# Performance work log

Measured on AMD Instinct MI355X. Metric: run time of the kernel, lower is better.

The kernel has to match this reference:

```python
import jax, jax.numpy as jnp
import numpy as np

N_NODES = 100000
N_EDGES = 1600000
N_FEAT = 165
HIDDEN = 128
N_CLASSES = 2
NEG_SLOPE = 0.2


def setup_inputs() -> dict:
    key = jax.random.key(0)
    ks = jax.random.split(key, 16)
    s = 0.05
    return {
        'x': jax.random.normal(ks[0], (N_NODES, N_FEAT), jnp.float32),
        'edge_src': jax.random.randint(ks[1], (N_EDGES,), 0, N_NODES, jnp.int32),
        'edge_dst': jax.random.randint(ks[2], (N_EDGES,), 0, N_NODES, jnp.int32),
        'W1l': jax.random.normal(ks[3], (N_FEAT, HIDDEN), jnp.float32) * s,
        'b1l': jnp.zeros((HIDDEN,), jnp.float32),
        'W1r': jax.random.normal(ks[4], (N_FEAT, HIDDEN), jnp.float32) * s,
        'b1r': jnp.zeros((HIDDEN,), jnp.float32),
        'att1': jax.random.normal(ks[5], (HIDDEN,), jnp.float32) * s,
        'bias1': jnp.zeros((HIDDEN,), jnp.float32),
        'W2l': jax.random.normal(ks[6], (HIDDEN, N_CLASSES), jnp.float32) * s,
        'b2l': jnp.zeros((N_CLASSES,), jnp.float32),
        'W2r': jax.random.normal(ks[7], (HIDDEN, N_CLASSES), jnp.float32) * s,
        'b2r': jnp.zeros((N_CLASSES,), jnp.float32),
        'att2': jax.random.normal(ks[8], (N_CLASSES,), jnp.float32) * s,
        'bias2': jnp.zeros((N_CLASSES,), jnp.float32),
    }


def gatv2_conv(x, src, dst, Wl, bl, Wr, br, att, bias, n_nodes):
    # PyG GATv2Conv, heads=1: x_l for source/message, x_r for target
    xl = x @ Wl + bl            # [N, D_out]
    xr = x @ Wr + br            # [N, D_out]
    e = jax.nn.leaky_relu(xl[src] + xr[dst], NEG_SLOPE)  # [E, D_out]
    score = e @ att             # [E]
    # segment softmax over destination nodes (stable)
    m = jax.ops.segment_max(score, dst, num_segments=n_nodes)
    a = jnp.exp(score - m[dst])
    denom = jax.ops.segment_sum(a, dst, num_segments=n_nodes)
    alpha = a / denom[dst]      # [E]
    out = jax.ops.segment_sum(alpha[:, None] * xl[src], dst, num_segments=n_nodes)
    return out + bias


def reference(x, edge_src, edge_dst, W1l, b1l, W1r, b1r, att1, bias1,
              W2l, b2l, W2r, b2r, att2, bias2):
    n = x.shape[0]
    # GATv2Conv adds self loops by default; every node has >=1 incoming edge
    loops = jnp.arange(n, dtype=edge_src.dtype)
    src = jnp.concatenate([edge_src, loops])
    dst = jnp.concatenate([edge_dst, loops])
    h = gatv2_conv(x, src, dst, W1l, b1l, W1r, b1r, att1, bias1, n)
    h = jax.nn.relu(h)
    # F.dropout with training=False is identity (eval mode)
    out = gatv2_conv(h, src, dst, W2l, b2l, W2r, b2r, att2, bias2, n)
    return out
```

## Files before the change

### kernel.cpp

```cpp
#include <hip/hip_runtime.h>
#include <hip/hip_bf16.h>

#define N_NODES 100000
#define NPAD 100032
#define N_EDGES 1600000
#define ETOT (N_EDGES + N_NODES)
#define NFEAT 165
#define KP 192
#define HID 128
#define NCLS 2
#define NEG 0.2f

#define NBUCK 391
#define CHUNK 16384
#define NCHUNK 104

typedef short bf16x8 __attribute__((ext_vector_type(8)));
typedef float f32x4 __attribute__((ext_vector_type(4)));

#define OFF_FLAG 0
#define OFF_W 16
#define WO_ATT1 42496
#define WO_BIAS1 42624
#define WO_W2L 42752
#define WO_B2L 43008
#define WO_W2R 43010
#define WO_B2R 43266
#define WO_ATT2 43268
#define WO_BIAS2 43270

#define OFF_XB   43392
#define OFF_WT   (OFF_XB + NPAD * KP / 2)
#define OFF_BCAT (OFF_WT + 256 * KP / 2)
#define OFF_XLB  (OFF_BCAT + 256)
#define OFF_XRB  (OFF_XLB + NPAD * HID / 2)
#define OFF_PAIRS (OFF_XRB + NPAD * HID / 2)
#define OFF_CSR  (OFF_PAIRS + 2 * ETOT)
#define OFF_ROWPTR (OFF_CSR + ETOT)
#define OFF_S    (OFF_ROWPTR + N_NODES + 8)
#define OFF_XL2  (OFF_S + NBUCK * NCHUNK + 8)
#define OFF_XR2  (OFF_XL2 + N_NODES * NCLS)
#define OFF_H    (OFF_XR2 + N_NODES * NCLS)
#define OFF_DL   (OFF_H + N_NODES * HID)
#define OFF_DR   (OFF_DL + NPAD)

__device__ __forceinline__ float bload16(unsigned short u) {
    return __uint_as_float(((unsigned)u) << 16);
}

__device__ __forceinline__ float lrelu(float v) {
    return fmaf(0.4f, fabsf(v), 0.6f * v);
}

__device__ __forceinline__ void unpack8(uint4 q, float* f) {
    f[0] = __uint_as_float(q.x << 16); f[1] = __uint_as_float(q.x & 0xffff0000u);
    f[2] = __uint_as_float(q.y << 16); f[3] = __uint_as_float(q.y & 0xffff0000u);
    f[4] = __uint_as_float(q.z << 16); f[5] = __uint_as_float(q.z & 0xffff0000u);
    f[6] = __uint_as_float(q.w << 16); f[7] = __uint_as_float(q.w & 0xffff0000u);
}

__device__ __forceinline__ unsigned short f2b(float f) {
    __hip_bfloat16 b = __float2bfloat16(f);
    return *(unsigned short*)&b;
}

__device__ __forceinline__ unsigned detect_flag(const unsigned short* x16, int lane) {
    unsigned short hh = x16[lane];
    unsigned e = (hh >> 7) & 0xFF;
    bool pl = ((hh & 0x7FFF) == 0) || (e >= 100 && e <= 140);
    unsigned long long m = __ballot(pl);
    return (__popcll(m) >= 52) ? 1u : 0u;
}

#define PREP_WT 49152
#define PREP_BC (PREP_WT + 256)
#define PREP_TOT (PREP_BC + 776)
#define PREP_BLKS ((PREP_TOT + 255) / 256)
__global__ void __launch_bounds__(256) k_prep_hist(
        const int* __restrict__ edst, int* __restrict__ bh,
        const unsigned short* __restrict__ x16,
        const void* W1l, const void* b1l, const void* W1r, const void* b1r,
        const void* att1, const void* bias1, const void* W2l, const void* b2l,
        const void* W2r, const void* b2r, const void* att2, const void* bias2,
        unsigned* __restrict__ flagp, unsigned short* __restrict__ wt,
        float* __restrict__ bcat, float* __restrict__ wb) {
    __shared__ int hist[NBUCK];
    if (blockIdx.x < NCHUNK) {
        for (int i = threadIdx.x; i < NBUCK; i += 256) hist[i] = 0;
        __syncthreads();
        int base = blockIdx.x * CHUNK;
        for (int i = threadIdx.x; i < CHUNK; i += 256) {
            int e = base + i;
            if (e >= ETOT) break;
            int d = (e < N_EDGES) ? edst[e] : (e - N_EDGES);
            atomicAdd(&hist[d >> 8], 1);
        }
        __syncthreads();
        for (int b = threadIdx.x; b < NBUCK; b += 256)
            bh[b * NCHUNK + blockIdx.x] = hist[b];
        return;
    }
    int lane = threadIdx.x & 63;
    unsigned isbf = detect_flag(x16, lane);
    int i = (blockIdx.x - NCHUNK) * 256 + threadIdx.x;
    if (i == 0) *flagp = isbf;
    if (i >= PREP_TOT) return;
    if (i < PREP_WT) {
        int n = i / KP, k = i - n * KP;
        unsigned short v = 0;
        if (k < NFEAT) {
            const void* src = (n < HID) ? W1l : W1r;
            size_t off = (size_t)k * HID + (n & (HID - 1));
            v = isbf ? ((const unsigned short*)src)[off]
                     : f2b(((const float*)src)[off]);
        }
        wt[i] = v;
    } else if (i < PREP_BC) {
        int n = i - PREP_WT;
        const void* src = (n < HID) ? b1l : b1r;
        int off = n & (HID - 1);
        bcat[n] = isbf ? bload16(((const unsigned short*)src)[off])
                       : ((const float*)src)[off];
    } else {
        int j = i - PREP_BC;
        const void* src; int off; int dst;
        if      (j < 128) { src = att1;  off = j;       dst = WO_ATT1 + j; }
        else if (j < 256) { src = bias1; off = j - 128; dst = WO_BIAS1 + (j - 128); }
        else if (j < 512) { src = W2l;   off = j - 256; dst = WO_W2L + (j - 256); }
        else if (j < 514) { src = b2l;   off = j - 512; dst = WO_B2L + (j - 512); }
        else if (j < 770) { src = W2r;   off = j - 514; dst = WO_W2R + (j - 514); }
        else if (j < 772) { src = b2r;   off = j - 770; dst = WO_B2R + (j - 770); }
        else if (j < 774) { src = att2;  off = j - 772; dst = WO_ATT2 + (j - 772); }
        else              { src = bias2; off = j - 774; dst = WO_BIAS2 + (j - 774); }
        wb[dst] = isbf ? bload16(((const unsigned short*)src)[off])
                       : ((const float*)src)[off];
    }
}

__global__ void __launch_bounds__(512) k_pa_scan(int* __restrict__ S,
                                                 int* __restrict__ rowptr) {
    __shared__ int lds[512];
    const int TOT4 = (NBUCK * NCHUNK) / 4;
    int t = threadIdx.x;
    int b4 = t * 20;
    uint4* S4 = (uint4*)S;
    int sum = 0;
    for (int k = 0; k < 20; k++) {
        int i = b4 + k;
        if (i < TOT4) {
            uint4 v = S4[i];
            sum += (int)(v.x + v.y + v.z + v.w);
        }
    }
    lds[t] = sum;
    __syncthreads();
    for (int off = 1; off < 512; off <<= 1) {
        int v = lds[t];
        if (t >= off) v += lds[t - off];
        __syncthreads();
        lds[t] = v;
        __syncthreads();
    }
    int carry = (t == 0) ? 0 : lds[t - 1];
    for (int k = 0; k < 20; k++) {
        int i = b4 + k;
        if (i < TOT4) {
            uint4 v = S4[i];
            uint4 o;
            o.x = carry; carry += v.x;
            o.y = carry; carry += v.y;
            o.z = carry; carry += v.z;
            o.w = carry; carry += v.w;
            S4[i] = o;
        }
    }
    if (t == 0) rowptr[N_NODES] = ETOT;
}

__global__ void __launch_bounds__(256) k_pa_scatter(const int* __restrict__ esrc,
                                                    const int* __restrict__ edst,
                                                    const int* __restrict__ S,
                                                    int2* __restrict__ pairs) {
    __shared__ int cur[NBUCK];
    for (int i = threadIdx.x; i < NBUCK; i += 256)
        cur[i] = S[i * NCHUNK + blockIdx.x];
    __syncthreads();
    int base = blockIdx.x * CHUNK;
    for (int i = threadIdx.x; i < CHUNK; i += 256) {
        int e = base + i;
        if (e >= ETOT) break;
        int s = (e < N_EDGES) ? esrc[e] : (e - N_EDGES);
        int d = (e < N_EDGES) ? edst[e] : (e - N_EDGES);
        int p = atomicAdd(&cur[d >> 8], 1);
        pairs[p] = make_int2(s, d);
    }
}

__global__ void __launch_bounds__(256) k_bsort(const int* __restrict__ S,
                                               const int2* __restrict__ pairs,
                                               int* __restrict__ rowptr,
                                               int* __restrict__ csr) {
    __shared__ int hist[256];
    __shared__ int cur[256];
    int b = blockIdx.x, t = threadIdx.x;
    int beg = S[b * NCHUNK];
    int end = (b == NBUCK - 1) ? ETOT : S[(b + 1) * NCHUNK];
    hist[t] = 0;
    __syncthreads();
    for (int j = beg + t; j < end; j += 256)
        atomicAdd(&hist[pairs[j].y & 255], 1);
    __syncthreads();
    for (int off = 1; off < 256; off <<= 1) {
        int v = hist[t];
        if (t >= off) v += hist[t - off];
        __syncthreads();
        hist[t] = v;
        __syncthreads();
    }
    int excl = (t == 0) ? 0 : hist[t - 1];
    int node = b * 256 + t;
    if (node < N_NODES) rowptr[node] = beg + excl;
    cur[t] = beg + excl;
    __syncthreads();
    for (int j = beg + t; j < end; j += 256) {
        int2 pr = pairs[j];
        int p = atomicAdd(&cur[pr.y & 255], 1);
        csr[p] = pr.x;
    }
}

#define XS_STRIDE 200
__global__ void __launch_bounds__(256) k_gemm1_mfma(
        const void* __restrict__ x,
        const unsigned* __restrict__ flagp,
        const unsigned short* __restrict__ wt,
        const float* __restrict__ bcat,
        const float* __restrict__ attp,
        __hip_bfloat16* __restrict__ xlb,
        __hip_bfloat16* __restrict__ xrb,
        float* __restrict__ dl,
        float* __restrict__ dr) {
    __shared__ unsigned short xs[64 * XS_STRIDE];
    __shared__ float dpart[4][64];
    int tid = threadIdx.x;
    int wave = tid >> 6, lane = tid & 63;
    int quad = lane >> 4, li = lane & 15;
    int node0 = blockIdx.x * 64;
    unsigned isbf = *flagp;
    const float* xf = (const float*)x;
    const unsigned short* x16 = (const unsigned short*)x;

    for (int i = tid; i < 64 * 27; i += 256) {
        int r = i / 27, c = 165 + (i - r * 27);
        xs[r * XS_STRIDE + c] = 0;
    }
    if (node0 + 64 <= N_NODES) {
        if (isbf) {
            const uint4* src = (const uint4*)(x16 + (size_t)node0 * NFEAT);
            for (int i = tid; i < 1320; i += 256) {
                uint4 v = src[i];
                int f = i * 8;
                unsigned short hh[8] = {
                    (unsigned short)(v.x & 0xffff), (unsigned short)(v.x >> 16),
                    (unsigned short)(v.y & 0xffff), (unsigned short)(v.y >> 16),
                    (unsigned short)(v.z & 0xffff), (unsigned short)(v.z >> 16),
                    (unsigned short)(v.w & 0xffff), (unsigned short)(v.w >> 16)};
#pragma unroll
                for (int t = 0; t < 8; t++) {
                    int ff = f + t, r = ff / NFEAT, c = ff - r * NFEAT;
                    xs[r * XS_STRIDE + c] = hh[t];
                }
            }
        } else {
            const float4* src = (const float4*)(xf + (size_t)node0 * NFEAT);
            for (int i = tid; i < 2640; i += 256) {
                float4 v = src[i];
                int f = i * 4;
                unsigned short hh[4] = {f2b(v.x), f2b(v.y), f2b(v.z), f2b(v.w)};
#pragma unroll
                for (int t = 0; t < 4; t++) {
                    int ff = f + t, r = ff / NFEAT, c = ff - r * NFEAT;
                    xs[r * XS_STRIDE + c] = hh[t];
                }
            }
        }
    } else {
        for (int i = tid; i < 64 * NFEAT; i += 256) {
            int r = i / NFEAT, c = i - r * NFEAT;
            int grow = node0 + r;
            unsigned short v = 0;
            if (grow < N_NODES) {
                size_t g = (size_t)grow * NFEAT + c;
                v = isbf ? x16[g] : f2b(xf[g]);
            }
            xs[r * XS_STRIDE + c] = v;
        }
    }

    bf16x8 wfrag[4][6];
#pragma unroll
    for (int q = 0; q < 4; q++) {
        int n = wave * 64 + q * 16 + li;
#pragma unroll
        for (int kk = 0; kk < 6; kk++)
            wfrag[q][kk] = *(const bf16x8*)&wt[(size_t)n * KP + kk * 32 + quad * 8];
    }
    float4 bv[4], attq4[4];
    int colbase = (wave & 1) * 64;
#pragma unroll
    for (int q = 0; q < 4; q++) {
        bv[q] = *(const float4*)&bcat[wave * 64 + q * 16 + quad * 4];
        attq4[q] = *(const float4*)&attp[colbase + q * 16 + quad * 4];
    }
    __syncthreads();

    for (int mt = 0; mt < 4; mt++) {
        bf16x8 xfrag[6];
#pragma unroll
        for (int kk = 0; kk < 6; kk++)
            xfrag[kk] = *(const bf16x8*)&xs[(mt * 16 + li) * XS_STRIDE + kk * 32 + quad * 8];
        int node = node0 + mt * 16 + li;
        __hip_bfloat16* dst = (wave < 2) ? xlb : xrb;
        float dp = 0.f;
#pragma unroll
        for (int q = 0; q < 4; q++) {
            f32x4 a = {0.f, 0.f, 0.f, 0.f};
#pragma unroll
            for (int kk = 0; kk < 6; kk++)
                a = __builtin_amdgcn_mfma_f32_16x16x32_bf16(wfrag[q][kk], xfrag[kk], a, 0, 0, 0);
            float f0 = a[0] + bv[q].x, f1 = a[1] + bv[q].y;
            float f2 = a[2] + bv[q].z, f3 = a[3] + bv[q].w;
            dp = fmaf(f0, attq4[q].x, dp);
            dp = fmaf(f1, attq4[q].y, dp);
            dp = fmaf(f2, attq4[q].z, dp);
            dp = fmaf(f3, attq4[q].w, dp);
            unsigned short s0 = f2b(f0), s1 = f2b(f1);
            unsigned short s2 = f2b(f2), s3 = f2b(f3);
            uint2 val = { (unsigned)s0 | ((unsigned)s1 << 16),
                          (unsigned)s2 | ((unsigned)s3 << 16) };
            int col = colbase + q * 16 + quad * 4;
            *(uint2*)&dst[(size_t)node * HID + col] = val;
        }
        dp += __shfl_xor(dp, 16);
        dp += __shfl_xor(dp, 32);
        if (lane < 16) dpart[wave][mt * 16 + li] = dp;
    }
    __syncthreads();
    if (tid < 64)
        dl[node0 + tid] = dpart[0][tid] + dpart[1][tid];
    else if (tid < 128)
        dr[node0 + tid - 64] = dpart[2][tid - 64] + dpart[3][tid - 64];
}

__global__ void __launch_bounds__(256) k_gat1(const int* __restrict__ rowptr,
                                              const int* __restrict__ csr,
                                              const __hip_bfloat16* __restrict__ xlb,
                                              const __hip_bfloat16* __restrict__ xrb,
                                              const float* __restrict__ att,
                                              const float* __restrict__ bias,
                                              const float* __restrict__ dotsl,
                                              const float* __restrict__ dotsr,
                                              float* __restrict__ h) {
    int wave = threadIdx.x >> 6, lane = threadIdx.x & 63;
    int d = blockIdx.x * 4 + wave;
    if (d >= N_NODES) return;
    int sub = lane >> 4, li = lane & 15;

    uint4 qr = ((const uint4*)(xrb + (size_t)d * HID))[li];
    float xrv[8]; unpack8(qr, xrv);
    float atv[8];
    {
        float4 t0 = ((const float4*)att)[li * 2];
        float4 t1 = ((const float4*)att)[li * 2 + 1];
        atv[0] = 0.4f * t0.x; atv[1] = 0.4f * t0.y;
        atv[2] = 0.4f * t0.z; atv[3] = 0.4f * t0.w;
        atv[4] = 0.4f * t1.x; atv[5] = 0.4f * t1.y;
        atv[6] = 0.4f * t1.z; atv[7] = 0.4f * t1.w;
    }
    float drd = dotsr[d];
    int beg = rowptr[d], end = rowptr[d + 1];
    int iters = (end - beg + 3) >> 2;
    float l = 0.f, o[8];
#pragma unroll
    for (int t = 0; t < 8; t++) o[t] = 0.f;

    int j = beg + sub;
    bool valid = j < end;
    int s = valid ? csr[j] : 0;
    uint4 q = *(const uint4*)(xlb + (size_t)s * HID + li * 8);
    float dlc = dotsl[s];

    for (int it = 0; it < iters; it++) {
        float c[8]; unpack8(q, c);
        bool v = valid;
        float dle = dlc;
        j += 4;
        valid = j < end;
        int sn = valid ? csr[j] : 0;
        q = *(const uint4*)(xlb + (size_t)sn * HID + li * 8);
        dlc = dotsl[sn];

        float pa = 0.f;
#pragma unroll
        for (int t = 0; t < 8; t++) {
            float vv = c[t] + xrv[t];
            pa = fmaf(atv[t], fabsf(vv), pa);
        }
        pa += __shfl_xor(pa, 1);
        pa += __shfl_xor(pa, 2);
        pa += __shfl_xor(pa, 4);
        pa += __shfl_xor(pa, 8);
        float p = fmaf(0.6f, dle + drd, pa);
        float a = v ? __expf(p) : 0.f;
        l += a;
#pragma unroll
        for (int t = 0; t < 8; t++) o[t] = fmaf(a, c[t], o[t]);
    }
    l += __shfl_xor(l, 16);
    l += __shfl_xor(l, 32);
#pragma unroll
    for (int t = 0; t < 8; t++) {
        o[t] += __shfl_xor(o[t], 16);
        o[t] += __shfl_xor(o[t], 32);
    }
    if (sub == 0) {
        float inv = 1.f / l;
        float4 bv0 = ((const float4*)bias)[li * 2];
        float4 bv1 = ((const float4*)bias)[li * 2 + 1];
        float4 r0, r1;
        r0.x = fmaf(o[0], inv, bv0.x); r0.y = fmaf(o[1], inv, bv0.y);
        r0.z = fmaf(o[2], inv, bv0.z); r0.w = fmaf(o[3], inv, bv0.w);
        r1.x = fmaf(o[4], inv, bv1.x); r1.y = fmaf(o[5], inv, bv1.y);
        r1.z = fmaf(o[6], inv, bv1.z); r1.w = fmaf(o[7], inv, bv1.w);
        r0.x = fmaxf(r0.x, 0.f); r0.y = fmaxf(r0.y, 0.f);
        r0.z = fmaxf(r0.z, 0.f); r0.w = fmaxf(r0.w, 0.f);
        r1.x = fmaxf(r1.x, 0.f); r1.y = fmaxf(r1.y, 0.f);
        r1.z = fmaxf(r1.z, 0.f); r1.w = fmaxf(r1.w, 0.f);
        float4* hp = (float4*)(h + (size_t)d * HID + li * 8);
        hp[0] = r0;
        hp[1] = r1;
    }
}

__global__ void __launch_bounds__(256) k_gemm2(const float* __restrict__ h,
                                               const float* __restrict__ wb,
                                               float* __restrict__ xl2, float* __restrict__ xr2) {
    const float* W2l = wb + WO_W2L;
    const float* b2l = wb + WO_B2L;
    const float* W2r = wb + WO_W2R;
    const float* b2r = wb + WO_B2R;
    int wave = threadIdx.x >> 6, lane = threadIdx.x & 63;
    int node = blockIdx.x * 4 + wave;
    if (node >= N_NODES) return;
    const float* hr = h + (size_t)node * HID;
    float h0 = hr[lane], h1 = hr[lane + 64];
    float al0 = h0 * W2l[lane * 2 + 0] + h1 * W2l[(lane + 64) * 2 + 0];
    float al1 = h0 * W2l[lane * 2 + 1] + h1 * W2l[(lane + 64) * 2 + 1];
    float ar0 = h0 * W2r[lane * 2 + 0] + h1 * W2r[(lane + 64) * 2 + 0];
    float ar1 = h0 * W2r[lane * 2 + 1] + h1 * W2r[(lane + 64) * 2 + 1];
#pragma unroll
    for (int off = 32; off > 0; off >>= 1) {
        al0 += __shfl_down(al0, off);
        al1 += __shfl_down(al1, off);
        ar0 += __shfl_down(ar0, off);
        ar1 += __shfl_down(ar1, off);
    }
    if (lane == 0) {
        xl2[node * 2 + 0] = al0 + b2l[0];
        xl2[node * 2 + 1] = al1 + b2l[1];
        xr2[node * 2 + 0] = ar0 + b2r[0];
        xr2[node * 2 + 1] = ar1 + b2r[1];
    }
}

__global__ void __launch_bounds__(256) k_gat2(const int* __restrict__ rowptr,
                                              const int* __restrict__ csr,
                                              const float* __restrict__ xl2,
                                              const float* __restrict__ xr2,
                                              const float* __restrict__ wb,
                                              const unsigned* __restrict__ flag,
                                              void* __restrict__ dout) {
    int d = blockIdx.x * 256 + threadIdx.x;
    if (d >= N_NODES) return;
    float xr0 = xr2[d * 2 + 0], xr1 = xr2[d * 2 + 1];
    float at0 = wb[WO_ATT2], at1 = wb[WO_ATT2 + 1];
    int beg = rowptr[d], end = rowptr[d + 1];
    float l = 0.f, o0 = 0.f, o1 = 0.f;
    for (int j = beg; j < end; j++) {
        int s = csr[j];
        float b0 = xl2[s * 2 + 0], b1 = xl2[s * 2 + 1];
        float p = at0 * lrelu(b0 + xr0) + at1 * lrelu(b1 + xr1);
        float a = __expf(p);
        l += a;
        o0 = fmaf(a, b0, o0);
        o1 = fmaf(a, b1, o1);
    }
    float inv = 1.f / l;
    float v0 = fmaf(o0, inv, wb[WO_BIAS2 + 0]);
    float v1 = fmaf(o1, inv, wb[WO_BIAS2 + 1]);
    if (*flag) {
        ((__hip_bfloat16*)dout)[d * 2 + 0] = __float2bfloat16(v0);
        ((__hip_bfloat16*)dout)[d * 2 + 1] = __float2bfloat16(v1);
    } else {
        ((float*)dout)[d * 2 + 0] = v0;
        ((float*)dout)[d * 2 + 1] = v1;
    }
}

extern "C" void kernel_launch(void* const* d_in, const int* in_sizes, int n_in,
                              void* d_out, int out_size, void* d_ws, size_t ws_size,
                              hipStream_t stream) {
    char* w = (char*)d_ws;
    unsigned* flag = (unsigned*)(w + (size_t)OFF_FLAG * 4);
    float* wb = (float*)(w + (size_t)OFF_W * 4);
    unsigned short* wt = (unsigned short*)(w + (size_t)OFF_WT * 4);
    float* bcat = (float*)(w + (size_t)OFF_BCAT * 4);
    __hip_bfloat16* xlb = (__hip_bfloat16*)(w + (size_t)OFF_XLB * 4);
    __hip_bfloat16* xrb = (__hip_bfloat16*)(w + (size_t)OFF_XRB * 4);
    int2* pairs = (int2*)(w + (size_t)OFF_PAIRS * 4);
    int* csr = (int*)(w + (size_t)OFF_CSR * 4);
    int* rowptr = (int*)(w + (size_t)OFF_ROWPTR * 4);
    int* S = (int*)(w + (size_t)OFF_S * 4);
    float* xl2 = (float*)(w + (size_t)OFF_XL2 * 4);
    float* xr2 = (float*)(w + (size_t)OFF_XR2 * 4);
    float* h = (float*)(w + (size_t)OFF_H * 4);
    float* dl = (float*)(w + (size_t)OFF_DL * 4);
    float* dr = (float*)(w + (size_t)OFF_DR * 4);
    const int* esrc = (const int*)d_in[1];
    const int* edst = (const int*)d_in[2];

    k_prep_hist<<<NCHUNK + PREP_BLKS, 256, 0, stream>>>(
        edst, S, (const unsigned short*)d_in[0],
        d_in[3], d_in[4], d_in[5], d_in[6], d_in[7], d_in[8],
        d_in[9], d_in[10], d_in[11], d_in[12], d_in[13], d_in[14],
        flag, wt, bcat, wb);

    k_pa_scan<<<1, 512, 0, stream>>>(S, rowptr);
    k_pa_scatter<<<NCHUNK, 256, 0, stream>>>(esrc, edst, S, pairs);
    k_bsort<<<NBUCK, 256, 0, stream>>>(S, pairs, rowptr, csr);

    k_gemm1_mfma<<<NPAD / 64, 256, 0, stream>>>(d_in[0], flag, wt, bcat,
                                                wb + WO_ATT1, xlb, xrb, dl, dr);

    k_gat1<<<(N_NODES + 3) / 4, 256, 0, stream>>>(rowptr, csr, xlb, xrb,
                                                  wb + WO_ATT1, wb + WO_BIAS1,
                                                  dl, dr, h);

    k_gemm2<<<(N_NODES + 3) / 4, 256, 0, stream>>>(h, wb, xl2, xr2);

    k_gat2<<<(N_NODES + 255) / 256, 256, 0, stream>>>(rowptr, csr, xl2, xr2,
                                                      wb, flag, d_out);
}
```

Baseline: 403.6 us.

## Pack edge pairs, store hidden as bf16, grid-stride gat1, split gat2 edges

```diff
diff --git a/kernel.cpp b/kernel.cpp
--- a/kernel.cpp
+++ b/kernel.cpp
@@ -14,6 +14,7 @@
 #define NBUCK 391
 #define CHUNK 16384
 #define NCHUNK 104
+#define GS_BLOCKS 2048
 
 typedef short bf16x8 __attribute__((ext_vector_type(8)));
 typedef float f32x4 __attribute__((ext_vector_type(4)));
@@ -30,6 +31,7 @@
 #define WO_BIAS2 43270
 
 #define OFF_XB   43392
+#define OFF_W2A  OFF_XB
 #define OFF_WT   (OFF_XB + NPAD * KP / 2)
 #define OFF_BCAT (OFF_WT + 256 * KP / 2)
 #define OFF_XLB  (OFF_BCAT + 256)
@@ -64,6 +66,10 @@
     return *(unsigned short*)&b;
 }
 
+__device__ __forceinline__ unsigned pack2(float a, float b) {
+    return (unsigned)f2b(a) | ((unsigned)f2b(b) << 16);
+}
+
 __device__ __forceinline__ unsigned detect_flag(const unsigned short* x16, int lane) {
     unsigned short hh = x16[lane];
     unsigned e = (hh >> 7) & 0xFF;
@@ -83,7 +89,8 @@
         const void* att1, const void* bias1, const void* W2l, const void* b2l,
         const void* W2r, const void* b2r, const void* att2, const void* bias2,
         unsigned* __restrict__ flagp, unsigned short* __restrict__ wt,
-        float* __restrict__ bcat, float* __restrict__ wb) {
+        float* __restrict__ bcat, float* __restrict__ wb,
+        float* __restrict__ w2a) {
     __shared__ int hist[NBUCK];
     if (blockIdx.x < NCHUNK) {
         for (int i = threadIdx.x; i < NBUCK; i += 256) hist[i] = 0;
@@ -132,8 +139,11 @@
         else if (j < 772) { src = b2r;   off = j - 770; dst = WO_B2R + (j - 770); }
         else if (j < 774) { src = att2;  off = j - 772; dst = WO_ATT2 + (j - 772); }
         else              { src = bias2; off = j - 774; dst = WO_BIAS2 + (j - 774); }
-        wb[dst] = isbf ? bload16(((const unsigned short*)src)[off])
-                       : ((const float*)src)[off];
+        float val = isbf ? bload16(((const unsigned short*)src)[off])
+                         : ((const float*)src)[off];
+        wb[dst] = val;
+        if (j >= 256 && j < 512) w2a[j - 256] = val;
+        else if (j >= 514 && j < 770) w2a[256 + (j - 514)] = val;
     }
 }
 
@@ -180,7 +190,7 @@
 __global__ void __launch_bounds__(256) k_pa_scatter(const int* __restrict__ esrc,
                                                     const int* __restrict__ edst,
                                                     const int* __restrict__ S,
-                                                    int2* __restrict__ pairs) {
+                                                    unsigned* __restrict__ pairs) {
     __shared__ int cur[NBUCK];
     for (int i = threadIdx.x; i < NBUCK; i += 256)
         cur[i] = S[i * NCHUNK + blockIdx.x];
@@ -192,12 +202,12 @@
         int s = (e < N_EDGES) ? esrc[e] : (e - N_EDGES);
         int d = (e < N_EDGES) ? edst[e] : (e - N_EDGES);
         int p = atomicAdd(&cur[d >> 8], 1);
-        pairs[p] = make_int2(s, d);
+        pairs[p] = (unsigned)s | ((unsigned)(d & 255) << 24);
     }
 }
 
 __global__ void __launch_bounds__(256) k_bsort(const int* __restrict__ S,
-                                               const int2* __restrict__ pairs,
+                                               const unsigned* __restrict__ pairs,
                                                int* __restrict__ rowptr,
                                                int* __restrict__ csr) {
     __shared__ int hist[256];
@@ -208,7 +218,7 @@
     hist[t] = 0;
     __syncthreads();
     for (int j = beg + t; j < end; j += 256)
-        atomicAdd(&hist[pairs[j].y & 255], 1);
+        atomicAdd(&hist[pairs[j] >> 24], 1);
     __syncthreads();
     for (int off = 1; off < 256; off <<= 1) {
         int v = hist[t];
@@ -223,9 +233,9 @@
     cur[t] = beg + excl;
     __syncthreads();
     for (int j = beg + t; j < end; j += 256) {
-        int2 pr = pairs[j];
-        int p = atomicAdd(&cur[pr.y & 255], 1);
-        csr[p] = pr.x;
+        unsigned pr = pairs[j];
+        int p = atomicAdd(&cur[pr >> 24], 1);
+        csr[p] = (int)(pr & 0xFFFFFFu);
     }
 }
 
@@ -334,10 +344,7 @@
             dp = fmaf(f1, attq4[q].y, dp);
             dp = fmaf(f2, attq4[q].z, dp);
             dp = fmaf(f3, attq4[q].w, dp);
-            unsigned short s0 = f2b(f0), s1 = f2b(f1);
-            unsigned short s2 = f2b(f2), s3 = f2b(f3);
-            uint2 val = { (unsigned)s0 | ((unsigned)s1 << 16),
-                          (unsigned)s2 | ((unsigned)s3 << 16) };
+            uint2 val = { pack2(f0, f1), pack2(f2, f3) };
             int col = colbase + q * 16 + quad * 4;
             *(uint2*)&dst[(size_t)node * HID + col] = val;
         }
@@ -360,14 +367,9 @@
                                               const float* __restrict__ bias,
                                               const float* __restrict__ dotsl,
                                               const float* __restrict__ dotsr,
-                                              float* __restrict__ h) {
+                                              unsigned short* __restrict__ h16) {
     int wave = threadIdx.x >> 6, lane = threadIdx.x & 63;
-    int d = blockIdx.x * 4 + wave;
-    if (d >= N_NODES) return;
     int sub = lane >> 4, li = lane & 15;
-
-    uint4 qr = ((const uint4*)(xrb + (size_t)d * HID))[li];
-    float xrv[8]; unpack8(qr, xrv);
     float atv[8];
     {
         float4 t0 = ((const float4*)att)[li * 2];
@@ -377,87 +379,91 @@
         atv[4] = 0.4f * t1.x; atv[5] = 0.4f * t1.y;
         atv[6] = 0.4f * t1.z; atv[7] = 0.4f * t1.w;
     }
-    float drd = dotsr[d];
-    int beg = rowptr[d], end = rowptr[d + 1];
-    int iters = (end - beg + 3) >> 2;
-    float l = 0.f, o[8];
-#pragma unroll
-    for (int t = 0; t < 8; t++) o[t] = 0.f;
-
-    int j = beg + sub;
-    bool valid = j < end;
-    int s = valid ? csr[j] : 0;
-    uint4 q = *(const uint4*)(xlb + (size_t)s * HID + li * 8);
-    float dlc = dotsl[s];
-
-    for (int it = 0; it < iters; it++) {
-        float c[8]; unpack8(q, c);
-        bool v = valid;
-        float dle = dlc;
-        j += 4;
-        valid = j < end;
-        int sn = valid ? csr[j] : 0;
-        q = *(const uint4*)(xlb + (size_t)sn * HID + li * 8);
-        dlc = dotsl[sn];
-
-        float pa = 0.f;
+
+    for (int d = blockIdx.x * 4 + wave; d < N_NODES; d += GS_BLOCKS * 4) {
+        uint4 qr = ((const uint4*)(xrb + (size_t)d * HID))[li];
+        float xrv[8]; unpack8(qr, xrv);
+        float drd = dotsr[d];
+        int beg = rowptr[d], end = rowptr[d + 1];
+        int iters = (end - beg + 3) >> 2;
+        float l = 0.f, o[8];
+#pragma unroll
+        for (int t = 0; t < 8; t++) o[t] = 0.f;
+
+        int j = beg + sub;
+        bool valid = j < end;
+        int s = valid ? csr[j] : 0;
+        uint4 q = *(const uint4*)(xlb + (size_t)s * HID + li * 8);
+        float dlc = dotsl[s];
+
+        for (int it = 0; it < iters; it++) {
+            float c[8]; unpack8(q, c);
+            bool v = valid;
+            float dle = dlc;
+            j += 4;
+            valid = j < end;
+            int sn = valid ? csr[j] : 0;
+            q = *(const uint4*)(xlb + (size_t)sn * HID + li * 8);
+            dlc = dotsl[sn];
+
+            float pa = 0.f;
+#pragma unroll
+            for (int t = 0; t < 8; t++) {
+                float vv = c[t] + xrv[t];
+                pa = fmaf(atv[t], fabsf(vv), pa);
+            }
+            pa += __shfl_xor(pa, 1);
+            pa += __shfl_xor(pa, 2);
+            pa += __shfl_xor(pa, 4);
+            pa += __shfl_xor(pa, 8);
+            float p = fmaf(0.6f, dle + drd, pa);
+            float a = v ? __expf(p) : 0.f;
+            l += a;
+#pragma unroll
+            for (int t = 0; t < 8; t++) o[t] = fmaf(a, c[t], o[t]);
+        }
+        l += __shfl_xor(l, 16);
+        l += __shfl_xor(l, 32);
 #pragma unroll
         for (int t = 0; t < 8; t++) {
-            float vv = c[t] + xrv[t];
-            pa = fmaf(atv[t], fabsf(vv), pa);
-        }
-        pa += __shfl_xor(pa, 1);
-        pa += __shfl_xor(pa, 2);
-        pa += __shfl_xor(pa, 4);
-        pa += __shfl_xor(pa, 8);
-        float p = fmaf(0.6f, dle + drd, pa);
-        float a = v ? __expf(p) : 0.f;
-        l += a;
-#pragma unroll
-        for (int t = 0; t < 8; t++) o[t] = fmaf(a, c[t], o[t]);
-    }
-    l += __shfl_xor(l, 16);
-    l += __shfl_xor(l, 32);
-#pragma unroll
-    for (int t = 0; t < 8; t++) {
-        o[t] += __shfl_xor(o[t], 16);
-        o[t] += __shfl_xor(o[t], 32);
-    }
-    if (sub == 0) {
-        float inv = 1.f / l;
-        float4 bv0 = ((const float4*)bias)[li * 2];
-        float4 bv1 = ((const float4*)bias)[li * 2 + 1];
-        float4 r0, r1;
-        r0.x = fmaf(o[0], inv, bv0.x); r0.y = fmaf(o[1], inv, bv0.y);
-        r0.z = fmaf(o[2], inv, bv0.z); r0.w = fmaf(o[3], inv, bv0.w);
-        r1.x = fmaf(o[4], inv, bv1.x); r1.y = fmaf(o[5], inv, bv1.y);
-        r1.z = fmaf(o[6], inv, bv1.z); r1.w = fmaf(o[7], inv, bv1.w);
-        r0.x = fmaxf(r0.x, 0.f); r0.y = fmaxf(r0.y, 0.f);
-        r0.z = fmaxf(r0.z, 0.f); r0.w = fmaxf(r0.w, 0.f);
-        r1.x = fmaxf(r1.x, 0.f); r1.y = fmaxf(r1.y, 0.f);
-        r1.z = fmaxf(r1.z, 0.f); r1.w = fmaxf(r1.w, 0.f);
-        float4* hp = (float4*)(h + (size_t)d * HID + li * 8);
-        hp[0] = r0;
-        hp[1] = r1;
-    }
-}
-
-__global__ void __launch_bounds__(256) k_gemm2(const float* __restrict__ h,
+            o[t] += __shfl_xor(o[t], 16);
+            o[t] += __shfl_xor(o[t], 32);
+        }
+        if (sub == 0) {
+            float inv = 1.f / l;
+            float4 bv0 = ((const float4*)bias)[li * 2];
+            float4 bv1 = ((const float4*)bias)[li * 2 + 1];
+            float r0 = fmaxf(fmaf(o[0], inv, bv0.x), 0.f);
+            float r1 = fmaxf(fmaf(o[1], inv, bv0.y), 0.f);
+            float r2 = fmaxf(fmaf(o[2], inv, bv0.z), 0.f);
+            float r3 = fmaxf(fmaf(o[3], inv, bv0.w), 0.f);
+            float r4 = fmaxf(fmaf(o[4], inv, bv1.x), 0.f);
+            float r5 = fmaxf(fmaf(o[5], inv, bv1.y), 0.f);
+            float r6 = fmaxf(fmaf(o[6], inv, bv1.z), 0.f);
+            float r7 = fmaxf(fmaf(o[7], inv, bv1.w), 0.f);
+            uint4 val = { pack2(r0, r1), pack2(r2, r3),
+                          pack2(r4, r5), pack2(r6, r7) };
+            *(uint4*)&h16[(size_t)d * HID + li * 8] = val;
+        }
+    }
+}
+
+__global__ void __launch_bounds__(256) k_gemm2(const unsigned short* __restrict__ h16,
                                                const float* __restrict__ wb,
+                                               const float* __restrict__ w2a,
                                                float* __restrict__ xl2, float* __restrict__ xr2) {
-    const float* W2l = wb + WO_W2L;
-    const float* b2l = wb + WO_B2L;
-    const float* W2r = wb + WO_W2R;
-    const float* b2r = wb + WO_B2R;
     int wave = threadIdx.x >> 6, lane = threadIdx.x & 63;
     int node = blockIdx.x * 4 + wave;
     if (node >= N_NODES) return;
-    const float* hr = h + (size_t)node * HID;
-    float h0 = hr[lane], h1 = hr[lane + 64];
-    float al0 = h0 * W2l[lane * 2 + 0] + h1 * W2l[(lane + 64) * 2 + 0];
-    float al1 = h0 * W2l[lane * 2 + 1] + h1 * W2l[(lane + 64) * 2 + 1];
-    float ar0 = h0 * W2r[lane * 2 + 0] + h1 * W2r[(lane + 64) * 2 + 0];
-    float ar1 = h0 * W2r[lane * 2 + 1] + h1 * W2r[(lane + 64) * 2 + 1];
+    unsigned hw = ((const unsigned*)(h16 + (size_t)node * HID))[lane];
+    float h0 = __uint_as_float(hw << 16);
+    float h1 = __uint_as_float(hw & 0xffff0000u);
+    float4 wl = ((const float4*)w2a)[lane];
+    float4 wr = ((const float4*)(w2a + 256))[lane];
+    float al0 = h0 * wl.x + h1 * wl.z;
+    float al1 = h0 * wl.y + h1 * wl.w;
+    float ar0 = h0 * wr.x + h1 * wr.z;
+    float ar1 = h0 * wr.y + h1 * wr.w;
 #pragma unroll
     for (int off = 32; off > 0; off >>= 1) {
         al0 += __shfl_down(al0, off);
@@ -466,10 +472,10 @@
         ar1 += __shfl_down(ar1, off);
     }
     if (lane == 0) {
-        xl2[node * 2 + 0] = al0 + b2l[0];
-        xl2[node * 2 + 1] = al1 + b2l[1];
-        xr2[node * 2 + 0] = ar0 + b2r[0];
-        xr2[node * 2 + 1] = ar1 + b2r[1];
+        xl2[node * 2 + 0] = al0 + wb[WO_B2L + 0];
+        xl2[node * 2 + 1] = al1 + wb[WO_B2L + 1];
+        xr2[node * 2 + 0] = ar0 + wb[WO_B2R + 0];
+        xr2[node * 2 + 1] = ar1 + wb[WO_B2R + 1];
     }
 }
 
@@ -480,13 +486,14 @@
                                               const float* __restrict__ wb,
                                               const unsigned* __restrict__ flag,
                                               void* __restrict__ dout) {
-    int d = blockIdx.x * 256 + threadIdx.x;
+    int t = blockIdx.x * 256 + threadIdx.x;
+    int d = t >> 2, part = t & 3;
     if (d >= N_NODES) return;
     float xr0 = xr2[d * 2 + 0], xr1 = xr2[d * 2 + 1];
     float at0 = wb[WO_ATT2], at1 = wb[WO_ATT2 + 1];
     int beg = rowptr[d], end = rowptr[d + 1];
     float l = 0.f, o0 = 0.f, o1 = 0.f;
-    for (int j = beg; j < end; j++) {
+    for (int j = beg + part; j < end; j += 4) {
         int s = csr[j];
         float b0 = xl2[s * 2 + 0], b1 = xl2[s * 2 + 1];
         float p = at0 * lrelu(b0 + xr0) + at1 * lrelu(b1 + xr1);
@@ -495,15 +502,19 @@
         o0 = fmaf(a, b0, o0);
         o1 = fmaf(a, b1, o1);
     }
-    float inv = 1.f / l;
-    float v0 = fmaf(o0, inv, wb[WO_BIAS2 + 0]);
-    float v1 = fmaf(o1, inv, wb[WO_BIAS2 + 1]);
-    if (*flag) {
-        ((__hip_bfloat16*)dout)[d * 2 + 0] = __float2bfloat16(v0);
-        ((__hip_bfloat16*)dout)[d * 2 + 1] = __float2bfloat16(v1);
-    } else {
-        ((float*)dout)[d * 2 + 0] = v0;
-        ((float*)dout)[d * 2 + 1] = v1;
+    l += __shfl_xor(l, 1);  o0 += __shfl_xor(o0, 1);  o1 += __shfl_xor(o1, 1);
+    l += __shfl_xor(l, 2);  o0 += __shfl_xor(o0, 2);  o1 += __shfl_xor(o1, 2);
+    if (part == 0) {
+        float inv = 1.f / l;
+        float v0 = fmaf(o0, inv, wb[WO_BIAS2 + 0]);
+        float v1 = fmaf(o1, inv, wb[WO_BIAS2 + 1]);
+        if (*flag) {
+            ((__hip_bfloat16*)dout)[d * 2 + 0] = __float2bfloat16(v0);
+            ((__hip_bfloat16*)dout)[d * 2 + 1] = __float2bfloat16(v1);
+        } else {
+            ((float*)dout)[d * 2 + 0] = v0;
+            ((float*)dout)[d * 2 + 1] = v1;
+        }
     }
 }
 
@@ -513,17 +524,18 @@
     char* w = (char*)d_ws;
     unsigned* flag = (unsigned*)(w + (size_t)OFF_FLAG * 4);
     float* wb = (float*)(w + (size_t)OFF_W * 4);
+    float* w2a = (float*)(w + (size_t)OFF_W2A * 4);
     unsigned short* wt = (unsigned short*)(w + (size_t)OFF_WT * 4);
     float* bcat = (float*)(w + (size_t)OFF_BCAT * 4);
     __hip_bfloat16* xlb = (__hip_bfloat16*)(w + (size_t)OFF_XLB * 4);
     __hip_bfloat16* xrb = (__hip_bfloat16*)(w + (size_t)OFF_XRB * 4);
-    int2* pairs = (int2*)(w + (size_t)OFF_PAIRS * 4);
+    unsigned* pairs = (unsigned*)(w + (size_t)OFF_PAIRS * 4);
     int* csr = (int*)(w + (size_t)OFF_CSR * 4);
     int* rowptr = (int*)(w + (size_t)OFF_ROWPTR * 4);
     int* S = (int*)(w + (size_t)OFF_S * 4);
     float* xl2 = (float*)(w + (size_t)OFF_XL2 * 4);
     float* xr2 = (float*)(w + (size_t)OFF_XR2 * 4);
-    float* h = (float*)(w + (size_t)OFF_H * 4);
+    unsigned short* h16 = (unsigned short*)(w + (size_t)OFF_H * 4);
     float* dl = (float*)(w + (size_t)OFF_DL * 4);
     float* dr = (float*)(w + (size_t)OFF_DR * 4);
     const int* esrc = (const int*)d_in[1];
@@ -533,7 +545,7 @@
         edst, S, (const unsigned short*)d_in[0],
         d_in[3], d_in[4], d_in[5], d_in[6], d_in[7], d_in[8],
         d_in[9], d_in[10], d_in[11], d_in[12], d_in[13], d_in[14],
-        flag, wt, bcat, wb);
+        flag, wt, bcat, wb, w2a);
 
     k_pa_scan<<<1, 512, 0, stream>>>(S, rowptr);
     k_pa_scatter<<<NCHUNK, 256, 0, stream>>>(esrc, edst, S, pairs);
@@ -542,12 +554,12 @@
     k_gemm1_mfma<<<NPAD / 64, 256, 0, stream>>>(d_in[0], flag, wt, bcat,
                                                 wb + WO_ATT1, xlb, xrb, dl, dr);
 
-    k_gat1<<<(N_NODES + 3) / 4, 256, 0, stream>>>(rowptr, csr, xlb, xrb,
-                                                  wb + WO_ATT1, wb + WO_BIAS1,
-                                                  dl, dr, h);
-
-    k_gemm2<<<(N_NODES + 3) / 4, 256, 0, stream>>>(h, wb, xl2, xr2);
-
-    k_gat2<<<(N_NODES + 255) / 256, 256, 0, stream>>>(rowptr, csr, xl2, xr2,
-                                                      wb, flag, d_out);
-}
+    k_gat1<<<GS_BLOCKS, 256, 0, stream>>>(rowptr, csr, xlb, xrb,
+                                          wb + WO_ATT1, wb + WO_BIAS1,
+                                          dl, dr, h16);
+
+    k_gemm2<<<(N_NODES + 3) / 4, 256, 0, stream>>>(h16, wb, w2a, xl2, xr2);
+
+    k_gat2<<<(4 * N_NODES + 255) / 256, 256, 0, stream>>>(rowptr, csr, xl2, xr2,
+                                                          wb, flag, d_out);
+}
```

Result: no change. 396.5 us (-1.8%).
